# Kernel optimization log

Measured on AMD Instinct MI355X. Metric: run time of the kernel, lower is better.

Reference implementation:

```python
import jax, jax.numpy as jnp
import numpy as np

B, N, C = 8, 1024, 768
H = 12
DH = C // H  # 64
FF = 3072
EPS = 1e-5


def _layer_norm(x, gamma, beta):
    mu = jnp.mean(x, axis=-1, keepdims=True)
    var = jnp.mean(jnp.square(x - mu), axis=-1, keepdims=True)
    return (x - mu) * jax.lax.rsqrt(var + EPS) * gamma + beta


def setup_inputs() -> dict:
    key = jax.random.key(0)
    ks = jax.random.split(key, 16)
    s_in = 1.0 / np.sqrt(C)
    s_ff = 1.0 / np.sqrt(FF)
    return {
        "x": jax.random.normal(ks[0], (B, N, C), dtype=jnp.float32),
        "Wq": jax.random.uniform(ks[1], (C, C), jnp.float32, -s_in, s_in),
        "bq": jax.random.uniform(ks[2], (C,), jnp.float32, -s_in, s_in),
        "Wk": jax.random.uniform(ks[3], (C, C), jnp.float32, -s_in, s_in),
        "bk": jax.random.uniform(ks[4], (C,), jnp.float32, -s_in, s_in),
        "Wv": jax.random.uniform(ks[5], (C, C), jnp.float32, -s_in, s_in),
        "bv": jax.random.uniform(ks[6], (C,), jnp.float32, -s_in, s_in),
        "Wo": jax.random.uniform(ks[7], (C, C), jnp.float32, -s_in, s_in),
        "bo": jax.random.uniform(ks[8], (C,), jnp.float32, -s_in, s_in),
        "g1": jnp.ones((C,), jnp.float32),
        "b1": jnp.zeros((C,), jnp.float32),
        "g2": jnp.ones((C,), jnp.float32),
        "b2": jnp.zeros((C,), jnp.float32),
        "W1": jax.random.uniform(ks[9], (C, FF), jnp.float32, -s_in, s_in),
        "bf1": jax.random.uniform(ks[10], (FF,), jnp.float32, -s_in, s_in),
        "W2": jax.random.uniform(ks[11], (FF, C), jnp.float32, -s_ff, s_ff),
        "bf2": jax.random.uniform(ks[12], (C,), jnp.float32, -s_ff, s_ff),
    }


def reference(x, Wq, bq, Wk, bk, Wv, bv, Wo, bo, g1, b1, g2, b2, W1, bf1, W2, bf2):
    # Pre-norm attention block
    xn = _layer_norm(x, g1, b1)
    q = (xn @ Wq + bq).reshape(B, N, H, DH)
    k = (xn @ Wk + bk).reshape(B, N, H, DH)
    v = (xn @ Wv + bv).reshape(B, N, H, DH)
    scores = jnp.einsum("bqhd,bkhd->bhqk", q, k) / np.sqrt(DH)  # [B,H,N,N]
    attn = jax.nn.softmax(scores, axis=-1)
    z = jnp.einsum("bhqk,bkhd->bqhd", attn, v).reshape(B, N, C)
    attn_out = z @ Wo + bo
    b = x + attn_out  # dropout is identity (p=0 / eval)
    # Pre-norm MLP block
    bn = _layer_norm(b, g2, b2)
    h = jax.nn.relu(bn @ W1 + bf1)
    y = b + (h @ W2 + bf2)
    return y
```

## Files before the change

### kernel.cpp

```cpp
#include <hip/hip_runtime.h>
#include <hip/hip_bf16.h>

#define BDIM 8
#define SEQ  1024
#define CH   768
#define NHD  12
#define DHD  64
#define FFD  3072
#define MR   (BDIM*SEQ)

typedef __attribute__((ext_vector_type(8))) short bf16x8;
typedef __attribute__((ext_vector_type(4))) float f32x4;
typedef unsigned int   u32;
typedef unsigned short u16;

__device__ __forceinline__ u16 f2bfu(float x) {
  __hip_bfloat16 h = __float2bfloat16(x);
  return *reinterpret_cast<u16*>(&h);
}

__device__ __forceinline__ void glds16(const void* g, void* l) {
  __builtin_amdgcn_global_load_lds(
      (const __attribute__((address_space(1))) u32*)g,
      (__attribute__((address_space(3))) u32*)l, 16, 0, 0);
}

__global__ __launch_bounds__(256) void k_transpose_all(
    const float* __restrict__ Wq, const float* __restrict__ Wk,
    const float* __restrict__ Wv, const float* __restrict__ Wo,
    const float* __restrict__ W1, const float* __restrict__ W2,
    u16* __restrict__ ws, const float* __restrict__ bq,
    const float* __restrict__ bk, const float* __restrict__ bv,
    float* __restrict__ bdst) {
  __shared__ float tile[32][33];
  int b = blockIdx.x;
  if (b >= 6912) {
    int i = (b - 6912) * 256 + threadIdx.x;
    if (i < 3 * CH)
      bdst[i] = i < CH ? bq[i] : (i < 2 * CH ? bk[i - CH] : bv[i - 2 * CH]);
    return;
  }
  int id, tb;
  if (b < 2304)      { id = b / 576; tb = b % 576; }
  else if (b < 4608) { id = 4;       tb = b - 2304; }
  else               { id = 5;       tb = b - 4608; }
  const float* src;
  u16* dst;
  int K, Nc;
  switch (id) {
    case 0: src = Wq; dst = ws;                      K = CH;  Nc = CH;  break;
    case 1: src = Wk; dst = ws + (size_t)CH*CH;      K = CH;  Nc = CH;  break;
    case 2: src = Wv; dst = ws + (size_t)2*CH*CH;    K = CH;  Nc = CH;  break;
    case 3: src = Wo; dst = ws + (size_t)3*CH*CH;    K = CH;  Nc = CH;  break;
    case 4: src = W1; dst = ws + (size_t)4*CH*CH;    K = CH;  Nc = FFD; break;
    default:src = W2; dst = ws + (size_t)4*CH*CH + (size_t)CH*FFD;
                                                     K = FFD; Nc = CH;  break;
  }
  int tilesx = Nc >> 5;
  int bx = (tb % tilesx) * 32;
  int by = (tb / tilesx) * 32;
  int tx = threadIdx.x & 31, ty = threadIdx.x >> 5;
#pragma unroll
  for (int j = 0; j < 32; j += 8)
    tile[ty + j][tx] = src[(size_t)(by + ty + j) * Nc + bx + tx];
  __syncthreads();
#pragma unroll
  for (int j = 0; j < 32; j += 8)
    dst[(size_t)(bx + ty + j) * K + by + tx] = f2bfu(tile[tx][ty + j]);
}

__global__ __launch_bounds__(256) void k_layernorm_bf16(
    const float* __restrict__ src, const float* __restrict__ gamma,
    const float* __restrict__ beta, u16* __restrict__ dst) {
  int row  = blockIdx.x * 4 + (threadIdx.x >> 6);
  int lane = threadIdx.x & 63;
  const float4* p4 = (const float4*)(src + (size_t)row * CH);
  float4 v[3];
  float s = 0.f, s2 = 0.f;
#pragma unroll
  for (int k = 0; k < 3; k++) {
    v[k] = p4[lane + k * 64];
    s  += v[k].x + v[k].y + v[k].z + v[k].w;
    s2 += v[k].x * v[k].x + v[k].y * v[k].y + v[k].z * v[k].z + v[k].w * v[k].w;
  }
#pragma unroll
  for (int m = 1; m < 64; m <<= 1) {
    s  += __shfl_xor(s,  m, 64);
    s2 += __shfl_xor(s2, m, 64);
  }
  float mean = s * (1.f / CH);
  float var  = s2 * (1.f / CH) - mean * mean;
  float rs   = rsqrtf(var + 1e-5f);
  u16* drow = dst + (size_t)row * CH;
#pragma unroll
  for (int k = 0; k < 3; k++) {
    int col = lane * 4 + k * 256;
    float4 gq = ((const float4*)gamma)[lane + k * 64];
    float4 bq = ((const float4*)beta )[lane + k * 64];
    u32 lo = (u32)f2bfu((v[k].x - mean) * rs * gq.x + bq.x) |
             ((u32)f2bfu((v[k].y - mean) * rs * gq.y + bq.y) << 16);
    u32 hi = (u32)f2bfu((v[k].z - mean) * rs * gq.z + bq.z) |
             ((u32)f2bfu((v[k].w - mean) * rs * gq.w + bq.w) << 16);
    uint2 w; w.x = lo; w.y = hi;
    *(uint2*)(drow + col) = w;
  }
}

enum { EPI_QKV = 0, EPI_RESID = 1, EPI_RELU = 2 };

template <int EPI>
__device__ __forceinline__ void gemm_epi(const f32x4& a, int row0, int col,
                                         float bval, const float* resid,
                                         void* outp, int Nmat) {
  if constexpr (EPI == EPI_QKV) {
    int sel = col / CH;
    int c = col - sel * CH;
    int h = c >> 6, d = c & 63;
    int bb = row0 >> 10, nn0 = row0 & (SEQ - 1);
    if (sel == 2) {
      union { uint2 u; u16 h4[4]; } pk;
#pragma unroll
      for (int r = 0; r < 4; r++) pk.h4[r] = f2bfu(a[r] + bval);
      *(uint2*)&((u16*)outp)[(size_t)2 * MR * CH +
                             (((size_t)(bb * NHD + h)) * DHD + d) * SEQ + nn0] =
          pk.u;
    } else {
#pragma unroll
      for (int r = 0; r < 4; r++)
        ((u16*)outp)[(size_t)sel * MR * CH +
                     (((size_t)(bb * NHD + h)) * SEQ + nn0 + r) * DHD + d] =
            f2bfu(a[r] + bval);
    }
  } else if constexpr (EPI == EPI_RESID) {
#pragma unroll
    for (int r = 0; r < 4; r++) {
      size_t idx = (size_t)(row0 + r) * Nmat + col;
      ((float*)outp)[idx] = a[r] + bval + resid[idx];
    }
  } else {
#pragma unroll
    for (int r = 0; r < 4; r++) {
      float val = a[r] + bval;
      ((u16*)outp)[(size_t)(row0 + r) * Nmat + col] =
          f2bfu(val > 0.f ? val : 0.f);
    }
  }
}

template <int EPI>
__global__ __launch_bounds__(256, 2) void k_gemmk64(
    const u16* __restrict__ A, const u16* __restrict__ Bt,
    const float* __restrict__ bias, const float* __restrict__ resid,
    void* __restrict__ outp, int K, int Nmat) {
  __shared__ u16 As[2][64 * 64];
  __shared__ u16 Bs[2][128 * 64];
  int tid = threadIdx.x;
  int bm = blockIdx.x, bn = blockIdx.y;
  int lane = tid & 63, wid = tid >> 6;
  int wr = (wid >> 1) * 32, wc = (wid & 1) * 64;
  int lrow = lane & 15, g = lane >> 4;

  const u16* Abase = A + (size_t)(bm * 64) * K;
  const u16* Bbase = Bt + (size_t)(bn * 128) * K;

  auto stage = [&](int buf, int k0) {
#pragma unroll
    for (int r = 0; r < 2; r++) {
      int u = tid + r * 256;
      int row = u >> 3, slot = u & 7;
      glds16(Abase + (size_t)row * K + k0 + ((slot ^ (row & 7)) << 3),
             &As[buf][u * 8]);
    }
#pragma unroll
    for (int r = 0; r < 4; r++) {
      int u = tid + r * 256;
      int row = u >> 3, slot = u & 7;
      glds16(Bbase + (size_t)row * K + k0 + ((slot ^ (row & 7)) << 3),
             &Bs[buf][u * 8]);
    }
  };

  int sx = lrow & 7;
  int x0 = (g ^ sx) * 8;
  int x1 = ((4 + g) ^ sx) * 8;

  f32x4 acc[2][4];
#pragma unroll
  for (int m = 0; m < 2; m++)
#pragma unroll
    for (int n = 0; n < 4; n++) acc[m][n] = {0.f, 0.f, 0.f, 0.f};

  int nk = K >> 6;
  stage(0, 0);
  for (int kt = 0; kt < nk; ++kt) {
    int buf = kt & 1;
    __syncthreads();
    if (kt + 1 < nk) stage(buf ^ 1, (kt + 1) << 6);
#pragma unroll
    for (int ks = 0; ks < 2; ks++) {
      int xs = ks ? x1 : x0;
      bf16x8 af[2], bfr[4];
#pragma unroll
      for (int m = 0; m < 2; m++)
        af[m] = *(const bf16x8*)&As[buf][(wr + m * 16 + lrow) * 64 + xs];
#pragma unroll
      for (int n = 0; n < 4; n++)
        bfr[n] = *(const bf16x8*)&Bs[buf][(wc + n * 16 + lrow) * 64 + xs];
      __builtin_amdgcn_s_setprio(1);
#pragma unroll
      for (int m = 0; m < 2; m++)
#pragma unroll
        for (int n = 0; n < 4; n++)
          acc[m][n] = __builtin_amdgcn_mfma_f32_16x16x32_bf16(
              af[m], bfr[n], acc[m][n], 0, 0, 0);
      __builtin_amdgcn_s_setprio(0);
    }
  }

#pragma unroll
  for (int m = 0; m < 2; m++) {
    int row0 = bm * 64 + wr + m * 16 + g * 4;
#pragma unroll
    for (int n = 0; n < 4; n++) {
      int col = bn * 128 + wc + n * 16 + lrow;
      gemm_epi<EPI>(acc[m][n], row0, col, bias[col], resid, outp, Nmat);
    }
  }
}

__global__ __launch_bounds__(512, 4) void k_attn(
    const u16* __restrict__ Q, const u16* __restrict__ Kk,
    const u16* __restrict__ Vt, u16* __restrict__ Z) {
  __shared__ u16 Ks[2][64 * 64];
  __shared__ u16 Vs[2][64 * 64];
  __shared__ u32 Psu[8][64 * 9];
  int tid = threadIdx.x, lane = tid & 63, wid = tid >> 6;
  int lrow = lane & 15, g = lane >> 4;
  int id  = blockIdx.x;
  int nid = (id & 7) * 96 + (id >> 3);
  int bh = nid >> 3;
  int qtile = (nid & 7) * 128;
  size_t base = (size_t)bh * SEQ * DHD;
  int bb = bh / NHD, hh = bh % NHD;
  int qrow0 = qtile + wid * 16;

  bf16x8 qf[2];
#pragma unroll
  for (int ks = 0; ks < 2; ks++)
    qf[ks] = *(const bf16x8*)(Q + base + (size_t)(qrow0 + lrow) * DHD +
                              ks * 32 + g * 8);

  f32x4 accO[4];
  float mrun = -1e30f, lrun = 0.f;
#pragma unroll
  for (int n = 0; n < 4; n++) accO[n] = {0.f, 0.f, 0.f, 0.f};

  int srow = tid >> 3;
  int swz  = (((tid & 7) * 16) ^ ((srow & 7) << 4)) >> 1;
  const u16* kg0 = Kk + base + (size_t)srow * DHD + swz;
  const u16* vg0 = Vt + base + (size_t)srow * SEQ + swz;

  auto stageKV = [&](int buf, int t) {
    glds16(kg0 + (size_t)t * 64 * DHD, &Ks[buf][tid * 8]);
    glds16(vg0 + t * 64,               &Vs[buf][tid * 8]);
  };

  int rc0 = ((g * 16)      ^ ((lrow & 7) << 4)) >> 1;
  int rc1 = ((64 + g * 16) ^ ((lrow & 7) << 4)) >> 1;

  stageKV(0, 0);
  for (int t = 0; t < 16; ++t) {
    int buf = t & 1;
    __syncthreads();
    if (t + 1 < 16) stageKV(buf ^ 1, t + 1);

    f32x4 sacc[4];
    __builtin_amdgcn_s_setprio(1);
#pragma unroll
    for (int n = 0; n < 4; n++) {
      bf16x8 kf0 = *(const bf16x8*)&Ks[buf][(n * 16 + lrow) * 64 + rc0];
      bf16x8 kf1 = *(const bf16x8*)&Ks[buf][(n * 16 + lrow) * 64 + rc1];
      sacc[n] = {0.f, 0.f, 0.f, 0.f};
      sacc[n] = __builtin_amdgcn_mfma_f32_16x16x32_bf16(kf0, qf[0], sacc[n], 0, 0, 0);
      sacc[n] = __builtin_amdgcn_mfma_f32_16x16x32_bf16(kf1, qf[1], sacc[n], 0, 0, 0);
    }
    __builtin_amdgcn_s_setprio(0);

    float mx = fmaxf(fmaxf(fmaxf(sacc[0][0], sacc[0][1]),
                           fmaxf(sacc[0][2], sacc[0][3])),
                     fmaxf(fmaxf(sacc[1][0], sacc[1][1]),
                           fmaxf(sacc[1][2], sacc[1][3])));
    mx = fmaxf(mx, fmaxf(fmaxf(fmaxf(sacc[2][0], sacc[2][1]),
                               fmaxf(sacc[2][2], sacc[2][3])),
                         fmaxf(fmaxf(sacc[3][0], sacc[3][1]),
                               fmaxf(sacc[3][2], sacc[3][3]))));
    mx *= 0.125f;
    mx = fmaxf(mx, __shfl_xor(mx, 16, 64));
    mx = fmaxf(mx, __shfl_xor(mx, 32, 64));

    if (__all(mx <= mrun + 8.f)) {
      float psum = 0.f;
#pragma unroll
      for (int n = 0; n < 4; n++)
#pragma unroll
        for (int r = 0; r < 4; r++) {
          float p = __expf(sacc[n][r] * 0.125f - mrun);
          sacc[n][r] = p;
          psum += p;
        }
      psum += __shfl_xor(psum, 16, 64);
      psum += __shfl_xor(psum, 32, 64);
      lrun += psum;
    } else {
      float mnew = fmaxf(mrun, mx);
      float alpha = __expf(mrun - mnew);
      float psum = 0.f;
#pragma unroll
      for (int n = 0; n < 4; n++)
#pragma unroll
        for (int r = 0; r < 4; r++) {
          float p = __expf(sacc[n][r] * 0.125f - mnew);
          sacc[n][r] = p;
          psum += p;
        }
      psum += __shfl_xor(psum, 16, 64);
      psum += __shfl_xor(psum, 32, 64);
      lrun = lrun * alpha + psum;
      mrun = mnew;
#pragma unroll
      for (int r = 0; r < 4; r++) {
        float ar = __shfl(alpha, (lane & 48) | (g * 4 + r), 64);
#pragma unroll
        for (int n = 0; n < 4; n++) accO[n][r] *= ar;
      }
    }

#pragma unroll
    for (int n = 0; n < 4; n++) {
      u32 lo = (u32)f2bfu(sacc[n][0]) | ((u32)f2bfu(sacc[n][1]) << 16);
      u32 hi = (u32)f2bfu(sacc[n][2]) | ((u32)f2bfu(sacc[n][3]) << 16);
      Psu[wid][lane * 9 + 2 * n]     = lo;
      Psu[wid][lane * 9 + 2 * n + 1] = hi;
    }

    int laneA = lrow + ((g & 1) << 5);
    int laneB = laneA + 16;
    int nsel = g >> 1;
    __builtin_amdgcn_s_setprio(1);
#pragma unroll
    for (int ks = 0; ks < 2; ks++) {
      int nks = 2 * ks + nsel;
      union { bf16x8 v; u32 w[4]; } pk;
      pk.w[0] = Psu[wid][laneA * 9 + 2 * nks];
      pk.w[1] = Psu[wid][laneA * 9 + 2 * nks + 1];
      pk.w[2] = Psu[wid][laneB * 9 + 2 * nks];
      pk.w[3] = Psu[wid][laneB * 9 + 2 * nks + 1];
      int rc = ks ? rc1 : rc0;
#pragma unroll
      for (int n = 0; n < 4; n++) {
        bf16x8 vf = *(const bf16x8*)&Vs[buf][(n * 16 + lrow) * 64 + rc];
        accO[n] = __builtin_amdgcn_mfma_f32_16x16x32_bf16(pk.v, vf,
                                                          accO[n], 0, 0, 0);
      }
    }
    __builtin_amdgcn_s_setprio(0);
  }

#pragma unroll
  for (int r = 0; r < 4; r++) {
    float lr = __shfl(lrun, (lane & 48) | (g * 4 + r), 64);
    float inv = 1.f / lr;
    int qrow = qrow0 + g * 4 + r;
#pragma unroll
    for (int n = 0; n < 4; n++) {
      int d = n * 16 + lrow;
      Z[((size_t)(bb * SEQ + qrow)) * CH + hh * DHD + d] =
          f2bfu(accO[n][r] * inv);
    }
  }
}

extern "C" void kernel_launch(void* const* d_in, const int* in_sizes, int n_in,
                              void* d_out, int out_size, void* d_ws,
                              size_t ws_size, hipStream_t stream) {
  (void)in_sizes; (void)n_in; (void)out_size; (void)ws_size;
  const float* x   = (const float*)d_in[0];
  const float* Wq  = (const float*)d_in[1];
  const float* bq  = (const float*)d_in[2];
  const float* Wk  = (const float*)d_in[3];
  const float* bk  = (const float*)d_in[4];
  const float* Wv  = (const float*)d_in[5];
  const float* bv  = (const float*)d_in[6];
  const float* Wo  = (const float*)d_in[7];
  const float* bo  = (const float*)d_in[8];
  const float* g1  = (const float*)d_in[9];
  const float* b1  = (const float*)d_in[10];
  const float* g2  = (const float*)d_in[11];
  const float* b2  = (const float*)d_in[12];
  const float* W1  = (const float*)d_in[13];
  const float* bf1 = (const float*)d_in[14];
  const float* W2  = (const float*)d_in[15];
  const float* bf2 = (const float*)d_in[16];

  u16* wsu  = (u16*)d_ws;
  u16* wq_t = wsu;
  u16* wo_t = wq_t + (size_t)3 * CH * CH;
  u16* w1_t = wo_t + (size_t)CH * CH;
  u16* w2_t = w1_t + (size_t)CH * FFD;
  u16* xn   = w2_t + (size_t)CH * FFD;
  u16* qb   = xn + (size_t)MR * CH;
  u16* zb   = qb + (size_t)3 * MR * CH;
  float* bres = (float*)(zb + (size_t)MR * CH);
  u16* hb   = qb;
  float* bqkv = (float*)d_out;

  dim3 blk(256);
  k_transpose_all<<<6921, blk, 0, stream>>>(Wq, Wk, Wv, Wo, W1, W2, wsu,
                                            bq, bk, bv, bqkv);

  k_layernorm_bf16<<<2048, blk, 0, stream>>>(x, g1, b1, xn);
  k_gemmk64<EPI_QKV><<<dim3(128, 18), blk, 0, stream>>>(
      xn, wq_t, bqkv, nullptr, qb, CH, 3 * CH);
  k_attn<<<768, dim3(512), 0, stream>>>(qb, qb + (size_t)MR * CH,
                                        qb + (size_t)2 * MR * CH, zb);
  k_gemmk64<EPI_RESID><<<dim3(128, 6), blk, 0, stream>>>(
      zb, wo_t, bo, x, bres, CH, CH);
  k_layernorm_bf16<<<2048, blk, 0, stream>>>(bres, g2, b2, xn);
  k_gemmk64<EPI_RELU><<<dim3(128, 24), blk, 0, stream>>>(
      xn, w1_t, bf1, nullptr, hb, CH, FFD);
  k_gemmk64<EPI_RESID><<<dim3(128, 6), blk, 0, stream>>>(
      hb, w2_t, bf2, bres, (float*)d_out, FFD, CH);
}
```

Baseline: 237.2 us.

## Fold softmax scale into Q, use exp2, compute row sums via MFMA

Pre-scales Q by log2(e)/sqrt(d) in the QKV epilogue so attention can use raw exp2 with no per-element multiply. The softmax row-sum is dropped from the VALU shuffle reductions and instead accumulated by an extra MFMA against a vector of bf16 ones. The max reduction is rewritten with three-input max chains. This trades VALU exp/reduction work for one more MFMA per k-step, and the denominator now sums the bf16-rounded probabilities.

```diff
diff --git a/kernel.cpp b/kernel.cpp
--- a/kernel.cpp
+++ b/kernel.cpp
@@ -13,6 +13,8 @@
 typedef __attribute__((ext_vector_type(4))) float f32x4;
 typedef unsigned int   u32;
 typedef unsigned short u16;
+
+#define QSCL 0.18033688f
 
 __device__ __forceinline__ u16 f2bfu(float x) {
   __hip_bfloat16 h = __float2bfloat16(x);
@@ -125,11 +127,12 @@
                              (((size_t)(bb * NHD + h)) * DHD + d) * SEQ + nn0] =
           pk.u;
     } else {
+      float scl = (sel == 0) ? QSCL : 1.f;
 #pragma unroll
       for (int r = 0; r < 4; r++)
         ((u16*)outp)[(size_t)sel * MR * CH +
                      (((size_t)(bb * NHD + h)) * SEQ + nn0 + r) * DHD + d] =
-            f2bfu(a[r] + bval);
+            f2bfu((a[r] + bval) * scl);
     }
   } else if constexpr (EPI == EPI_RESID) {
 #pragma unroll
@@ -250,8 +253,13 @@
     qf[ks] = *(const bf16x8*)(Q + base + (size_t)(qrow0 + lrow) * DHD +
                               ks * 32 + g * 8);
 
+  bf16x8 vone;
+#pragma unroll
+  for (int j = 0; j < 8; j++) vone[j] = (short)0x3F80;
+
   f32x4 accO[4];
-  float mrun = -1e30f, lrun = 0.f;
+  f32x4 accS = {0.f, 0.f, 0.f, 0.f};
+  float mrun = -1e30f;
 #pragma unroll
   for (int n = 0; n < 4; n++) accO[n] = {0.f, 0.f, 0.f, 0.f};
 
@@ -267,6 +275,8 @@
 
   int rc0 = ((g * 16)      ^ ((lrow & 7) << 4)) >> 1;
   int rc1 = ((64 + g * 16) ^ ((lrow & 7) << 4)) >> 1;
+
+  auto mx3 = [](float a, float b, float c) { return fmaxf(fmaxf(a, b), c); };
 
   stageKV(0, 0);
   for (int t = 0; t < 16; ++t) {
@@ -286,50 +296,34 @@
     }
     __builtin_amdgcn_s_setprio(0);
 
-    float mx = fmaxf(fmaxf(fmaxf(sacc[0][0], sacc[0][1]),
-                           fmaxf(sacc[0][2], sacc[0][3])),
-                     fmaxf(fmaxf(sacc[1][0], sacc[1][1]),
-                           fmaxf(sacc[1][2], sacc[1][3])));
-    mx = fmaxf(mx, fmaxf(fmaxf(fmaxf(sacc[2][0], sacc[2][1]),
-                               fmaxf(sacc[2][2], sacc[2][3])),
-                         fmaxf(fmaxf(sacc[3][0], sacc[3][1]),
-                               fmaxf(sacc[3][2], sacc[3][3]))));
-    mx *= 0.125f;
+    float a0 = mx3(sacc[0][0], sacc[0][1], sacc[0][2]);
+    float a1 = mx3(sacc[0][3], sacc[1][0], sacc[1][1]);
+    float a2 = mx3(sacc[1][2], sacc[1][3], sacc[2][0]);
+    float a3 = mx3(sacc[2][1], sacc[2][2], sacc[2][3]);
+    float a4 = mx3(sacc[3][0], sacc[3][1], sacc[3][2]);
+    float mx = fmaxf(mx3(a0, a1, a2), mx3(a3, a4, sacc[3][3]));
     mx = fmaxf(mx, __shfl_xor(mx, 16, 64));
     mx = fmaxf(mx, __shfl_xor(mx, 32, 64));
 
-    if (__all(mx <= mrun + 8.f)) {
-      float psum = 0.f;
+    if (__all(mx <= mrun + 11.54f)) {
 #pragma unroll
       for (int n = 0; n < 4; n++)
 #pragma unroll
-        for (int r = 0; r < 4; r++) {
-          float p = __expf(sacc[n][r] * 0.125f - mrun);
-          sacc[n][r] = p;
-          psum += p;
-        }
-      psum += __shfl_xor(psum, 16, 64);
-      psum += __shfl_xor(psum, 32, 64);
-      lrun += psum;
+        for (int r = 0; r < 4; r++)
+          sacc[n][r] = __builtin_amdgcn_exp2f(sacc[n][r] - mrun);
     } else {
       float mnew = fmaxf(mrun, mx);
-      float alpha = __expf(mrun - mnew);
-      float psum = 0.f;
+      float alpha = __builtin_amdgcn_exp2f(mrun - mnew);
 #pragma unroll
       for (int n = 0; n < 4; n++)
 #pragma unroll
-        for (int r = 0; r < 4; r++) {
-          float p = __expf(sacc[n][r] * 0.125f - mnew);
-          sacc[n][r] = p;
-          psum += p;
-        }
-      psum += __shfl_xor(psum, 16, 64);
-      psum += __shfl_xor(psum, 32, 64);
-      lrun = lrun * alpha + psum;
+        for (int r = 0; r < 4; r++)
+          sacc[n][r] = __builtin_amdgcn_exp2f(sacc[n][r] - mnew);
       mrun = mnew;
 #pragma unroll
       for (int r = 0; r < 4; r++) {
         float ar = __shfl(alpha, (lane & 48) | (g * 4 + r), 64);
+        accS[r] *= ar;
 #pragma unroll
         for (int n = 0; n < 4; n++) accO[n][r] *= ar;
       }
@@ -362,14 +356,14 @@
         accO[n] = __builtin_amdgcn_mfma_f32_16x16x32_bf16(pk.v, vf,
                                                           accO[n], 0, 0, 0);
       }
+      accS = __builtin_amdgcn_mfma_f32_16x16x32_bf16(pk.v, vone, accS, 0, 0, 0);
     }
     __builtin_amdgcn_s_setprio(0);
   }
 
 #pragma unroll
   for (int r = 0; r < 4; r++) {
-    float lr = __shfl(lrun, (lane & 48) | (g * 4 + r), 64);
-    float inv = 1.f / lr;
+    float inv = 1.f / accS[r];
     int qrow = qrow0 + g * 4 + r;
 #pragma unroll
     for (int n = 0; n < 4; n++) {
```

Result: no change. 234.2 us (-1.3%).
